# Kernel optimization log

Measured on AMD Instinct MI355X. Metric: run time of the kernel, lower is better.

The kernel has to match this reference:

```python
import jax, jax.numpy as jnp
import numpy as np

B, T, D, R, KEXP = 4, 4096, 1024, 64, 8
RH = max(D, 32)
SCALE = 0.02


def setup_inputs() -> dict:
    key = jax.random.key(0)
    ks = jax.random.split(key, 20)
    x = jax.random.normal(ks[0], (B, T, D), dtype=jnp.float32)
    W_Q = jax.random.normal(ks[1], (D, D), dtype=jnp.float32) * (1.0 / np.sqrt(D))
    W_K = jax.random.normal(ks[2], (D, D), dtype=jnp.float32) * (1.0 / np.sqrt(D))
    W_O = jax.random.normal(ks[3], (D, D), dtype=jnp.float32) * (1.0 / np.sqrt(D))
    W_inv = jnp.eye(D, dtype=jnp.float32) + 0.01 * jax.random.normal(ks[4], (D, D), dtype=jnp.float32)
    V_fwd = jax.random.normal(ks[5], (KEXP, D, R), dtype=jnp.float32) * SCALE
    W_fwd = jax.random.normal(ks[6], (KEXP, D, R), dtype=jnp.float32) * SCALE
    U_fwd = jax.random.normal(ks[7], (KEXP, D, R), dtype=jnp.float32) * SCALE
    b_fwd = jnp.zeros((KEXP, D), dtype=jnp.float32)
    V_inv = jax.random.normal(ks[8], (KEXP, D, R), dtype=jnp.float32) * SCALE
    W_inv_exp = jax.random.normal(ks[9], (KEXP, D, R), dtype=jnp.float32) * SCALE
    U_inv = jax.random.normal(ks[10], (KEXP, D, R), dtype=jnp.float32) * SCALE
    b_inv = jnp.zeros((KEXP, D), dtype=jnp.float32)
    router_w1 = jax.random.normal(ks[11], (RH, D), dtype=jnp.float32) * (1.0 / np.sqrt(D))
    router_b1 = jnp.zeros((RH,), dtype=jnp.float32)
    router_w2 = jax.random.normal(ks[12], (KEXP, RH), dtype=jnp.float32) * (1.0 / np.sqrt(RH))
    router_b2 = jnp.zeros((KEXP,), dtype=jnp.float32)
    alpha_bi = jnp.asarray(0.5, dtype=jnp.float32)
    expert_bias = jnp.zeros((KEXP,), dtype=jnp.float32)
    return dict(x=x, W_Q=W_Q, W_K=W_K, W_O=W_O, W_inv=W_inv,
                V_fwd=V_fwd, W_fwd=W_fwd, U_fwd=U_fwd, b_fwd=b_fwd,
                V_inv=V_inv, W_inv_exp=W_inv_exp, U_inv=U_inv, b_inv=b_inv,
                router_w1=router_w1, router_b1=router_b1,
                router_w2=router_w2, router_b2=router_b2,
                alpha_bi=alpha_bi, expert_bias=expert_bias)


def _fused_branch(Q_side, K_side, V, W, U, b, router_w1, router_b1, router_w2, router_b2, expert_bias):
    # Q_side, K_side: (B,T,D); V,W,U: (K,D,r); b: (K,D)
    xV = jnp.einsum('btd,kdr->btkr', Q_side, V)          # (B,T,K,r)
    yW = jnp.einsum('btd,kdr->btkr', K_side, W)          # (B,T,K,r)
    cum_yW = jnp.cumsum(yW, axis=1)                      # causal prefix sum over T
    prod = xV * cum_yW
    # query-side router: Linear -> GELU(exact) -> Linear, plus balance bias
    h = jax.nn.gelu(Q_side @ router_w1.T + router_b1, approximate=False)
    logits = h @ router_w2.T + router_b2 + expert_bias
    weights = jax.nn.softmax(logits, axis=-1)            # (B,T,K)
    out = jnp.einsum('btkr,kdr->btd', prod * weights[..., None], U)
    out = out + weights @ b
    n_valid = jnp.arange(1, Q_side.shape[1] + 1, dtype=Q_side.dtype)
    return out / n_valid[None, :, None]


def reference(x, W_Q, W_K, W_O, W_inv,
              V_fwd, W_fwd, U_fwd, b_fwd,
              V_inv, W_inv_exp, U_inv, b_inv,
              router_w1, router_b1, router_w2, router_b2,
              alpha_bi, expert_bias):
    Q = x @ W_Q.T
    K = x @ W_K.T
    invQ = Q @ W_inv.T
    invK = K @ W_inv.T
    fwd = _fused_branch(Q, K, V_fwd, W_fwd, U_fwd, b_fwd,
                        router_w1, router_b1, router_w2, router_b2, expert_bias)
    inv = _fused_branch(invQ, invK, W_inv_exp, V_inv, U_inv, b_inv,
                        router_w1, router_b1, router_w2, router_b2, expert_bias)
    out = fwd + alpha_bi * inv
    return out @ W_O.T
```

## Files before the change

kernel.cpp:

```cpp
#include <hip/hip_runtime.h>
#include <hip/hip_bf16.h>
#include <math.h>

#define BDIM 1024
#define TDIM 4096
#define BT   16384
#define KEXPN 8
#define RRANK 64
#define KR   512
#define KC   640
#define PW   1280
#define KRC  1024
#define NCH  64
#define TC   64

typedef __attribute__((ext_vector_type(8))) short bf16x8;
typedef __attribute__((ext_vector_type(4))) float f32x4;

typedef __attribute__((address_space(1))) char g_char;
typedef __attribute__((address_space(3))) char l_char;

__device__ __forceinline__ void gload16(const short* g, short* lds_base_uniform) {
  __builtin_amdgcn_global_load_lds((const g_char*)(const char*)g,
                                   (l_char*)(char*)lds_base_uniform, 16, 0, 0);
}

__global__ __launch_bounds__(256) void cvt_bf16_kernel(const float* __restrict__ in,
    __hip_bfloat16* __restrict__ out, long n4) {
  long id = (long)blockIdx.x * 256 + threadIdx.x;
  if (id >= n4) return;
  f32x4 v = ((const f32x4*)in)[id];
  long i = id * 4;
  out[i + 0] = __float2bfloat16(v[0]);
  out[i + 1] = __float2bfloat16(v[1]);
  out[i + 2] = __float2bfloat16(v[2]);
  out[i + 3] = __float2bfloat16(v[3]);
}

__global__ __launch_bounds__(256) void transpose3_kernel(
    const float* __restrict__ in0, __hip_bfloat16* __restrict__ o0,
    const float* __restrict__ in1, __hip_bfloat16* __restrict__ o1,
    const float* __restrict__ in2, __hip_bfloat16* __restrict__ o2) {
  int id = blockIdx.x * 256 + threadIdx.x;
  if (id >= BDIM * BDIM) return;
  const float* in = blockIdx.y == 0 ? in0 : (blockIdx.y == 1 ? in1 : in2);
  __hip_bfloat16* out = blockIdx.y == 0 ? o0 : (blockIdx.y == 1 ? o1 : o2);
  int d = id & (BDIM - 1);
  int e = id >> 10;
  out[(size_t)e * BDIM + d] = __float2bfloat16(in[(size_t)d * BDIM + e]);
}

__global__ __launch_bounds__(256) void vmat4_kernel(
    const float* __restrict__ i0, __hip_bfloat16* __restrict__ o0,
    const float* __restrict__ i1, __hip_bfloat16* __restrict__ o1,
    const float* __restrict__ i2, __hip_bfloat16* __restrict__ o2,
    const float* __restrict__ i3, __hip_bfloat16* __restrict__ o3) {
  int id = blockIdx.x * 256 + threadIdx.x;
  if (id >= KR * BDIM) return;
  const float* V = blockIdx.y == 0 ? i0 : (blockIdx.y == 1 ? i1 : (blockIdx.y == 2 ? i2 : i3));
  __hip_bfloat16* out = blockIdx.y == 0 ? o0 : (blockIdx.y == 1 ? o1 : (blockIdx.y == 2 ? o2 : o3));
  int d = id & (BDIM - 1);
  int kr = id >> 10;
  int k = kr >> 6, r = kr & 63;
  out[(size_t)kr * BDIM + d] = __float2bfloat16(V[((size_t)k * BDIM + d) * RRANK + r]);
}

__global__ __launch_bounds__(256) void utT2_kernel(
    const float* __restrict__ U0, const float* __restrict__ b0, __hip_bfloat16* __restrict__ o0,
    const float* __restrict__ U1, const float* __restrict__ b1, __hip_bfloat16* __restrict__ o1) {
  int id = blockIdx.x * 256 + threadIdx.x;
  if (id >= KC * BDIM) return;
  const float* U = blockIdx.y ? U1 : U0;
  const float* bvec = blockIdx.y ? b1 : b0;
  __hip_bfloat16* out = blockIdx.y ? o1 : o0;
  int e = id & (BDIM - 1);
  int c = id >> 10;
  float v = 0.0f;
  if (c < KR) {
    int k = c >> 6, r = c & 63;
    v = U[((size_t)k * BDIM + e) * RRANK + r];
  } else if (c < KR + KEXPN) {
    v = bvec[(size_t)(c - KR) * BDIM + e];
  }
  out[(size_t)c * BDIM + e] = __float2bfloat16(v);
}

__global__ __launch_bounds__(256) void gemm_fold(const __hip_bfloat16* __restrict__ A,
    const __hip_bfloat16* __restrict__ B, void* __restrict__ C1, void* __restrict__ C2,
    void* __restrict__ C3, int rs1, int rs2, int ldc, int M, int N, int Kd) {
  __shared__ __align__(16) short Als[2][128 * 32];
  __shared__ __align__(16) short Bls[2][128 * 32];
  int nbx = gridDim.x;
  int nwg = nbx * gridDim.y;
  int bx = blockIdx.x, by = blockIdx.y;
  if ((nwg & 7) == 0) {
    int orig = by * nbx + bx;
    int cpx = nwg >> 3;
    int id = (orig & 7) * cpx + (orig >> 3);
    bx = id % nbx; by = id / nbx;
  }
  const short* As = (const short*)A;
  const short* Bs = (const short*)B;
  const int t  = threadIdx.x;
  const int w  = t >> 6;
  const int l  = t & 63;
  const int lr = l & 15;
  const int lk = l >> 4;
  const int wr = w >> 1;
  const int wc = w & 1;
  const int row0 = by * 128;
  const int col0 = bx * 128;
  const int srow = w * 16 + (l >> 2);
  const int scol = (l & 3) * 8;
  const short* ag0 = As + (size_t)(row0 + srow) * Kd + scol;
  const short* ag1 = As + (size_t)(row0 + 64 + srow) * Kd + scol;
  const short* bg0 = Bs + (size_t)(col0 + srow) * Kd + scol;
  const short* bg1 = Bs + (size_t)(col0 + 64 + srow) * Kd + scol;
  f32x4 acc[4][4] = {};
  const int nt = Kd / 32;
  auto stage = [&](int kt, int buf) {
    int k0 = kt * 32;
    gload16(ag0 + k0, &Als[buf][w * 512]);
    gload16(ag1 + k0, &Als[buf][2048 + w * 512]);
    gload16(bg0 + k0, &Bls[buf][w * 512]);
    gload16(bg1 + k0, &Bls[buf][2048 + w * 512]);
  };
  stage(0, 0);
  __syncthreads();
  int cur = 0;
  for (int kt = 0; kt < nt; ++kt) {
    if (kt + 1 < nt) stage(kt + 1, cur ^ 1);
    bf16x8 af[4], bfr[4];
    #pragma unroll
    for (int i = 0; i < 4; i++)
      af[i] = *(const bf16x8*)&Als[cur][(wr * 64 + i * 16 + lr) * 32 + lk * 8];
    #pragma unroll
    for (int j = 0; j < 4; j++)
      bfr[j] = *(const bf16x8*)&Bls[cur][(wc * 64 + j * 16 + lr) * 32 + lk * 8];
    #pragma unroll
    for (int i = 0; i < 4; i++)
      #pragma unroll
      for (int j = 0; j < 4; j++)
        acc[i][j] = __builtin_amdgcn_mfma_f32_16x16x32_bf16(af[i], bfr[j], acc[i][j], 0, 0, 0);
    __syncthreads();
    cur ^= 1;
  }
  #pragma unroll
  for (int i = 0; i < 4; i++)
    #pragma unroll
    for (int j = 0; j < 4; j++)
      #pragma unroll
      for (int g = 0; g < 4; g++) {
        int r = row0 + wr * 64 + i * 16 + lk * 4 + g;
        int c = col0 + wc * 64 + j * 16 + lr;
        void* dst = C1; int rr = r;
        if (r >= rs2)      { dst = C3; rr = r - rs2; }
        else if (r >= rs1) { dst = C2; rr = r - rs1; }
        ((__hip_bfloat16*)dst)[(size_t)rr * ldc + c] = __float2bfloat16(acc[i][j][g]);
      }
}

template<int EPI>
__global__ __launch_bounds__(512, 2) void gemm_nt_256(const __hip_bfloat16* __restrict__ A,
    const __hip_bfloat16* __restrict__ B, void* __restrict__ Cv, void* __restrict__ Cv2,
    int csplit, int ldc, int ldc2, const float* __restrict__ bias, int M, int N, int Kd) {
  __shared__ __align__(16) short Als[2][2][256 * 32];
  __shared__ __align__(16) short Bls[2][2][256 * 32];

  int nbx = gridDim.x;
  int nwg = nbx * gridDim.y;
  int bx = blockIdx.x, by = blockIdx.y;
  if ((nwg & 7) == 0) {
    int orig = by * nbx + bx;
    int cpx = nwg >> 3;
    int id = (orig & 7) * cpx + (orig >> 3);
    bx = id % nbx; by = id / nbx;
  }
  const short* As = (const short*)A;
  const short* Bs = (const short*)B;
  const int t  = threadIdx.x;
  const int w  = t >> 6;
  const int l  = t & 63;
  const int lr = l & 15;
  const int lk = l >> 4;
  const int wr = w >> 2;
  const int wc = w & 3;
  const int row0 = by * 256;
  const int col0 = bx * 256;

  const int srow  = t >> 2;
  const int sslot = (t & 3) ^ ((srow >> 1) & 3);
  const short* agA0 = As + (size_t)(row0 + srow) * Kd + sslot * 8;
  const short* agA1 = As + (size_t)(row0 + 128 + srow) * Kd + sslot * 8;
  const short* bgB0 = Bs + (size_t)(col0 + srow) * Kd + sslot * 8;
  const short* bgB1 = Bs + (size_t)(col0 + 128 + srow) * Kd + sslot * 8;

  auto stageA = [&](int buf, int kh, int kt) {
    int k0 = kt * 64 + kh * 32;
    short* base = &Als[buf][kh][0];
    gload16(agA0 + k0, base + w * 512);
    gload16(agA1 + k0, base + 4096 + w * 512);
  };
  auto stageB = [&](int buf, int kh, int kt) {
    int k0 = kt * 64 + kh * 32;
    short* base = &Bls[buf][kh][0];
    gload16(bgB0 + k0, base + w * 512);
    gload16(bgB1 + k0, base + 4096 + w * 512);
  };

  int aoff[8], boff[4];
  #pragma unroll
  for (int mf = 0; mf < 8; ++mf) {
    int r = wr * 128 + mf * 16 + lr;
    aoff[mf] = r * 32 + ((lk ^ ((r >> 1) & 3)) << 3);
  }
  #pragma unroll
  for (int nf = 0; nf < 4; ++nf) {
    int r = wc * 64 + nf * 16 + lr;
    boff[nf] = r * 32 + ((lk ^ ((r >> 1) & 3)) << 3);
  }

  f32x4 acc[8][4] = {};
  const int NT = Kd >> 6;

  stageA(0, 0, 0); stageA(0, 1, 0); stageB(0, 0, 0); stageB(0, 1, 0);
  asm volatile("s_waitcnt vmcnt(0)" ::: "memory");
  __builtin_amdgcn_sched_barrier(0);
  __builtin_amdgcn_s_barrier();

  for (int kt = 0; kt < NT; ++kt) {
    const int buf = kt & 1, nb = buf ^ 1;
    const short* A0 = &Als[buf][0][0];
    const short* A1 = &Als[buf][1][0];
    const short* B0 = &Bls[buf][0][0];
    const short* B1 = &Bls[buf][1][0];
    const bool st = (kt + 1 < NT);
    bf16x8 af[4], bfr[4];

    #pragma unroll
    for (int i = 0; i < 4; ++i) bfr[i] = *(const bf16x8*)&B0[boff[i]];
    #pragma unroll
    for (int i = 0; i < 4; ++i) af[i]  = *(const bf16x8*)&A0[aoff[i]];
    if (st) { stageA(nb, 0, kt + 1); stageA(nb, 1, kt + 1); }
    __builtin_amdgcn_s_barrier();
    __builtin_amdgcn_s_setprio(1);
    #pragma unroll
    for (int i = 0; i < 4; ++i)
      #pragma unroll
      for (int j = 0; j < 4; ++j)
        acc[i][j] = __builtin_amdgcn_mfma_f32_16x16x32_bf16(af[i], bfr[j], acc[i][j], 0, 0, 0);
    __builtin_amdgcn_s_setprio(0);
    __builtin_amdgcn_s_barrier();

    #pragma unroll
    for (int i = 0; i < 4; ++i) af[i] = *(const bf16x8*)&A0[aoff[4 + i]];
    if (st) { stageB(nb, 0, kt + 1); stageB(nb, 1, kt + 1); }
    __builtin_amdgcn_s_barrier();
    __builtin_amdgcn_s_setprio(1);
    #pragma unroll
    for (int i = 0; i < 4; ++i)
      #pragma unroll
      for (int j = 0; j < 4; ++j)
        acc[4 + i][j] = __builtin_amdgcn_mfma_f32_16x16x32_bf16(af[i], bfr[j], acc[4 + i][j], 0, 0, 0);
    __builtin_amdgcn_s_setprio(0);
    __builtin_amdgcn_s_barrier();

    #pragma unroll
    for (int i = 0; i < 4; ++i) bfr[i] = *(const bf16x8*)&B1[boff[i]];
    #pragma unroll
    for (int i = 0; i < 4; ++i) af[i]  = *(const bf16x8*)&A1[aoff[i]];
    __builtin_amdgcn_s_barrier();
    __builtin_amdgcn_s_setprio(1);
    #pragma unroll
    for (int i = 0; i < 4; ++i)
      #pragma unroll
      for (int j = 0; j < 4; ++j)
        acc[i][j] = __builtin_amdgcn_mfma_f32_16x16x32_bf16(af[i], bfr[j], acc[i][j], 0, 0, 0);
    __builtin_amdgcn_s_setprio(0);
    __builtin_amdgcn_s_barrier();

    #pragma unroll
    for (int i = 0; i < 4; ++i) af[i] = *(const bf16x8*)&A1[aoff[4 + i]];
    __builtin_amdgcn_s_barrier();
    __builtin_amdgcn_s_setprio(1);
    #pragma unroll
    for (int i = 0; i < 4; ++i)
      #pragma unroll
      for (int j = 0; j < 4; ++j)
        acc[4 + i][j] = __builtin_amdgcn_mfma_f32_16x16x32_bf16(af[i], bfr[j], acc[4 + i][j], 0, 0, 0);
    __builtin_amdgcn_s_setprio(0);
    asm volatile("s_waitcnt vmcnt(0)" ::: "memory");
    __builtin_amdgcn_sched_barrier(0);
    __builtin_amdgcn_s_barrier();
  }

  #pragma unroll
  for (int mf = 0; mf < 8; ++mf)
    #pragma unroll
    for (int nf = 0; nf < 4; ++nf)
      #pragma unroll
      for (int g = 0; g < 4; ++g) {
        int r = row0 + wr * 128 + mf * 16 + lk * 4 + g;
        int c = col0 + wc * 64 + nf * 16 + lr;
        float v = acc[mf][nf][g];
        void* dst = Cv;
        int cc = c, ld = ldc;
        if (c >= csplit) { dst = Cv2; cc = c - csplit; ld = ldc2; }
        size_t idx = (size_t)r * ld + cc;
        if (EPI == 0)      ((float*)dst)[idx] = v;
        else if (EPI == 1) ((__hip_bfloat16*)dst)[idx] = __float2bfloat16(v);
        else if (EPI == 2) {
          float xv = v + bias[cc];
          float gl = 0.5f * xv * (1.0f + erff(xv * 0.70710678118654752f));
          ((__hip_bfloat16*)dst)[idx] = __float2bfloat16(gl);
        } else {
          float s = 1.0f / (float)((r & (TDIM - 1)) + 1);
          ((float*)dst)[idx] = v * s;
        }
      }
}

__global__ __launch_bounds__(256) void router_kernel(const __hip_bfloat16* __restrict__ Hf,
    const __hip_bfloat16* __restrict__ Hi,
    const float* __restrict__ w2, const float* __restrict__ b2,
    const float* __restrict__ ebias, float* __restrict__ wgt_f, float* __restrict__ wgt_i) {
  const __hip_bfloat16* H = blockIdx.y ? Hi : Hf;
  float* wgt = blockIdx.y ? wgt_i : wgt_f;
  int wv = threadIdx.x >> 6;
  int l  = threadIdx.x & 63;
  int row = blockIdx.x * 4 + wv;
  if (row >= BT) return;
  const short* Hs = (const short*)H;
  float acc[KEXPN] = {};
  #pragma unroll
  for (int i = 0; i < BDIM / 512; i++) {
    int h = (i * 64 + l) * 8;
    bf16x8 hv = *(const bf16x8*)(Hs + (size_t)row * BDIM + h);
    #pragma unroll
    for (int j = 0; j < 8; j++) {
      unsigned int ui = ((unsigned int)(unsigned short)hv[j]) << 16;
      float xv = __uint_as_float(ui);
      #pragma unroll
      for (int k = 0; k < KEXPN; k++) acc[k] += xv * w2[k * BDIM + h + j];
    }
  }
  #pragma unroll
  for (int k = 0; k < KEXPN; k++)
    for (int off = 32; off; off >>= 1) acc[k] += __shfl_down(acc[k], off);
  if (l == 0) {
    float lg[KEXPN];
    float mx = -1e30f;
    #pragma unroll
    for (int k = 0; k < KEXPN; k++) { lg[k] = acc[k] + b2[k] + ebias[k]; mx = fmaxf(mx, lg[k]); }
    float s = 0.0f;
    #pragma unroll
    for (int k = 0; k < KEXPN; k++) { lg[k] = expf(lg[k] - mx); s += lg[k]; }
    float inv = 1.0f / s;
    #pragma unroll
    for (int k = 0; k < KEXPN; k++) wgt[(size_t)row * KEXPN + k] = lg[k] * inv;
  }
}

__global__ __launch_bounds__(1024) void chunksum_kernel(const __hip_bfloat16* __restrict__ yW,
    float* __restrict__ S) {
  int j  = threadIdx.x;
  int ch = blockIdx.x;
  int b  = blockIdx.y;
  size_t base = ((size_t)b * TDIM + ch * TC) * KRC + j;
  float s = 0.0f;
  for (int t = 0; t < TC; t++) s += __bfloat162float(yW[base + (size_t)t * KRC]);
  S[((size_t)b * NCH + ch) * KRC + j] = s;
}

__global__ __launch_bounds__(1024) void scan_chunks_kernel(float* __restrict__ S) {
  int j = threadIdx.x;
  int b = blockIdx.x;
  float run = 0.0f;
  for (int ch = 0; ch < NCH; ch++) {
    size_t i = ((size_t)b * NCH + ch) * KRC + j;
    float v = S[i];
    S[i] = run;
    run += v;
  }
}

__global__ __launch_bounds__(1024) void combine_kernel(const __hip_bfloat16* __restrict__ yW,
    const float* __restrict__ S, const __hip_bfloat16* __restrict__ xV,
    const float* __restrict__ wf, const float* __restrict__ wi,
    const float* __restrict__ alphaPtr, __hip_bfloat16* __restrict__ P) {
  int j  = threadIdx.x;
  int ch = blockIdx.x;
  int b  = blockIdx.y;
  float alpha = alphaPtr[0];
  float scale = (j < KR) ? 1.0f : alpha;
  const float* wgt = (j < KR) ? wf : wi;
  int k = (j & (KR - 1)) >> 6;
  int pcol = (j < KR) ? j : j + 128;
  float run = S[((size_t)b * NCH + ch) * KRC + j];
  for (int t0 = 0; t0 < TC; t0++) {
    size_t row = (size_t)b * TDIM + ch * TC + t0;
    run += __bfloat162float(yW[row * KRC + j]);
    float p = __bfloat162float(xV[row * KRC + j]) * run * wgt[row * KEXPN + k] * scale;
    P[row * PW + pcol] = __float2bfloat16(p);
  }
  if (j < 256) {
    int half = j >> 7, jj = j & 127;
    int col = half ? (KC + KR + jj) : (KR + jj);
    const float* wg = half ? wi : wf;
    float sc = half ? alpha : 1.0f;
    for (int t0 = 0; t0 < TC; t0++) {
      size_t row = (size_t)b * TDIM + ch * TC + t0;
      float v = (jj < KEXPN) ? wg[row * KEXPN + jj] * sc : 0.0f;
      P[row * PW + col] = __float2bfloat16(v);
    }
  }
}

__global__ __launch_bounds__(256) void fill_kernel(float* __restrict__ out, long n, float val) {
  long id = (long)blockIdx.x * 256 + threadIdx.x;
  if (id < n) out[id] = val;
}

extern "C" void kernel_launch(void* const* d_in, const int* in_sizes, int n_in,
                              void* d_out, int out_size, void* d_ws, size_t ws_size,
                              hipStream_t stream) {
  const float* x        = (const float*)d_in[0];
  const float* W_Q      = (const float*)d_in[1];
  const float* W_K      = (const float*)d_in[2];
  const float* W_O      = (const float*)d_in[3];
  const float* W_inv    = (const float*)d_in[4];
  const float* V_fwd    = (const float*)d_in[5];
  const float* W_fwd    = (const float*)d_in[6];
  const float* U_fwd    = (const float*)d_in[7];
  const float* b_fwd    = (const float*)d_in[8];
  const float* V_inv    = (const float*)d_in[9];
  const float* W_inv_e  = (const float*)d_in[10];
  const float* U_inv    = (const float*)d_in[11];
  const float* b_inv    = (const float*)d_in[12];
  const float* rw1      = (const float*)d_in[13];
  const float* rb1      = (const float*)d_in[14];
  const float* rw2      = (const float*)d_in[15];
  const float* rb2      = (const float*)d_in[16];
  const float* alphaPtr = (const float*)d_in[17];
  const float* ebias    = (const float*)d_in[18];

  char* ws = (char*)d_ws;
  size_t off = 0;
  auto alloc = [&](size_t sz) -> void* {
    void* p = ws + off;
    off += (sz + 255) & ~(size_t)255;
    return p;
  };

  const size_t RB = (size_t)BDIM * 2;
  void* winvT = alloc((size_t)BDIM * RB);
  void* wqT   = alloc((size_t)BDIM * RB);
  void* wkT   = alloc((size_t)BDIM * RB);
  void* wo    = alloc((size_t)BDIM * RB);
  void* ST    = alloc((size_t)2048 * RB);
  void* HXQ   = alloc((size_t)3072 * RB);
  void* XKA   = alloc((size_t)1024 * RB);
  void* HWq   = alloc((size_t)2048 * RB);
  void* XYW   = alloc((size_t)2048 * RB);
  void* UTT   = alloc((size_t)1280 * RB);
  void* Mcat  = alloc((size_t)BDIM * PW * 2);
  void* wgt_f = alloc((size_t)BT * KEXPN * 4);
  void* wgt_i = alloc((size_t)BT * KEXPN * 4);
  void* S     = alloc((size_t)4 * NCH * KRC * 4);
  void* s_x   = alloc((size_t)BT * BDIM * 2);
  void* Hf    = alloc((size_t)BT * BDIM * 2);
  void* Hi    = alloc((size_t)BT * BDIM * 2);
  void* xVcat = alloc((size_t)BT * KRC * 2);
  void* yWcat = alloc((size_t)BT * KRC * 2);
  void* Pcat  = Hf;

  if (off > ws_size) {
    fill_kernel<<<dim3((unsigned)((out_size + 255) / 256)), 256, 0, stream>>>(
        (float*)d_out, (long)out_size, (float)(off >> 20));
    return;
  }

  __hip_bfloat16* STp  = (__hip_bfloat16*)ST;
  __hip_bfloat16* HXQp = (__hip_bfloat16*)HXQ;
  __hip_bfloat16* XKAp = (__hip_bfloat16*)XKA;
  __hip_bfloat16* XYWp = (__hip_bfloat16*)XYW;
  __hip_bfloat16* UTTp = (__hip_bfloat16*)UTT;

  auto cvt = [&](const float* in, void* out, long n) {
    long n4 = n / 4;
    cvt_bf16_kernel<<<dim3((unsigned)((n4 + 255) / 256)), dim3(256), 0, stream>>>(
        in, (__hip_bfloat16*)out, n4);
  };
  auto fold = [&](const void* A, const void* Bm, void* C1, void* C2, void* C3,
                  int rs1, int rs2, int ldc, int M, int N, int Kd) {
    dim3 g(N / 128, M / 128);
    gemm_fold<<<g, 256, 0, stream>>>((const __hip_bfloat16*)A, (const __hip_bfloat16*)Bm,
        C1, C2, C3, rs1, rs2, ldc, M, N, Kd);
  };
  auto gemm2b = [&](const void* A, const void* Bm, void* C, void* C2, int csplit,
                    int ldc, int ldc2, int M, int N, int Kd, int epi, const float* bias) {
    dim3 g(N / 256, M / 256);
    if (epi == 1)      gemm_nt_256<1><<<g, 512, 0, stream>>>((const __hip_bfloat16*)A, (const __hip_bfloat16*)Bm, C, C2, csplit, ldc, ldc2, bias, M, N, Kd);
    else if (epi == 2) gemm_nt_256<2><<<g, 512, 0, stream>>>((const __hip_bfloat16*)A, (const __hip_bfloat16*)Bm, C, C2, csplit, ldc, ldc2, bias, M, N, Kd);
    else               gemm_nt_256<4><<<g, 512, 0, stream>>>((const __hip_bfloat16*)A, (const __hip_bfloat16*)Bm, C, C2, csplit, ldc, ldc2, bias, M, N, Kd);
  };

  cvt(x,   s_x, (long)BT * BDIM);
  cvt(W_O, wo,  (long)BDIM * BDIM);
  cvt(rw1, STp,  (long)BDIM * BDIM);
  cvt(rw1, HXQp, (long)BDIM * BDIM);
  transpose3_kernel<<<dim3((BDIM * BDIM + 255) / 256, 3), 256, 0, stream>>>(
      W_inv, (__hip_bfloat16*)winvT, W_Q, (__hip_bfloat16*)wqT, W_K, (__hip_bfloat16*)wkT);
  vmat4_kernel<<<dim3((KR * BDIM + 255) / 256, 4), 256, 0, stream>>>(
      V_fwd,   HXQp + (size_t)2048 * BDIM,
      W_fwd,   XKAp,
      W_inv_e, STp + (size_t)1024 * BDIM,
      V_inv,   STp + (size_t)1536 * BDIM);
  utT2_kernel<<<dim3((KC * BDIM + 255) / 256, 2), 256, 0, stream>>>(
      U_fwd, b_fwd, UTTp, U_inv, b_inv, UTTp + (size_t)KC * BDIM);

  fold(ST, winvT, HXQp + (size_t)1024 * BDIM, HXQp + (size_t)2560 * BDIM,
       XKAp + (size_t)512 * BDIM, 1024, 1536, BDIM, 2048, BDIM, BDIM);
  fold(HXQ, wqT, HWq, XYWp, XYWp, 2048, 4096, BDIM, 3072, BDIM, BDIM);
  fold(XKA, wkT, XYWp + (size_t)1024 * BDIM, nullptr, nullptr, 1024, 2048, BDIM, 1024, BDIM, BDIM);
  fold(wo, UTT, Mcat, nullptr, nullptr, 1024, 2048, PW, BDIM, PW, BDIM);

  gemm2b(s_x, HWq, Hf, Hi, BDIM, BDIM, BDIM, BT, 2 * BDIM, BDIM, 2, rb1);
  gemm2b(s_x, XYW, xVcat, yWcat, BDIM, BDIM, BDIM, BT, 2 * BDIM, BDIM, 1, nullptr);

  router_kernel<<<dim3(BT / 4, 2), 256, 0, stream>>>((const __hip_bfloat16*)Hf,
      (const __hip_bfloat16*)Hi, rw2, rb2, ebias, (float*)wgt_f, (float*)wgt_i);

  dim3 gch(NCH, 4);
  chunksum_kernel<<<gch, 1024, 0, stream>>>((const __hip_bfloat16*)yWcat, (float*)S);
  scan_chunks_kernel<<<dim3(4), 1024, 0, stream>>>((float*)S);
  combine_kernel<<<gch, 1024, 0, stream>>>((const __hip_bfloat16*)yWcat, (const float*)S,
      (const __hip_bfloat16*)xVcat, (const float*)wgt_f, (const float*)wgt_i,
      alphaPtr, (__hip_bfloat16*)Pcat);

  gemm2b(Pcat, Mcat, d_out, d_out, BDIM, BDIM, BDIM, BT, BDIM, PW, 4, nullptr);
}
```

Baseline: 464.0 us.

## Merge fold GEMMs into paired launches and fuse x-side GEMMs into one

The four small weight-folding GEMMs are grouped into two launches, each running two independent problems over a shared flat grid. The two large x-side GEMMs (router hidden and the xV/yW projections) become one GEMM with N=4096 and a four-way segmented epilogue that applies GELU only to the first two segments. The P/Mcat layout is also compacted from 1280 to 1152 columns by packing both branches' bias-weight columns together, which shrinks the final GEMM's K dimension. This cuts launch count and padded work, at the cost of a more branchy epilogue.

```diff
diff --git a/kernel.cpp b/kernel.cpp
--- a/kernel.cpp
+++ b/kernel.cpp
@@ -8,8 +8,7 @@
 #define KEXPN 8
 #define RRANK 64
 #define KR   512
-#define KC   640
-#define PW   1280
+#define PW2  1152
 #define KRC  1024
 #define NCH  64
 #define TC   64
@@ -65,42 +64,41 @@
   out[(size_t)kr * BDIM + d] = __float2bfloat16(V[((size_t)k * BDIM + d) * RRANK + r]);
 }
 
-__global__ __launch_bounds__(256) void utT2_kernel(
-    const float* __restrict__ U0, const float* __restrict__ b0, __hip_bfloat16* __restrict__ o0,
-    const float* __restrict__ U1, const float* __restrict__ b1, __hip_bfloat16* __restrict__ o1) {
+__global__ __launch_bounds__(256) void utt_pack_kernel(
+    const float* __restrict__ Uf, const float* __restrict__ bf,
+    const float* __restrict__ Ui, const float* __restrict__ bi,
+    __hip_bfloat16* __restrict__ out) {
   int id = blockIdx.x * 256 + threadIdx.x;
-  if (id >= KC * BDIM) return;
-  const float* U = blockIdx.y ? U1 : U0;
-  const float* bvec = blockIdx.y ? b1 : b0;
-  __hip_bfloat16* out = blockIdx.y ? o1 : o0;
+  if (id >= PW2 * BDIM) return;
   int e = id & (BDIM - 1);
   int c = id >> 10;
   float v = 0.0f;
   if (c < KR) {
     int k = c >> 6, r = c & 63;
-    v = U[((size_t)k * BDIM + e) * RRANK + r];
-  } else if (c < KR + KEXPN) {
-    v = bvec[(size_t)(c - KR) * BDIM + e];
+    v = Uf[((size_t)k * BDIM + e) * RRANK + r];
+  } else if (c < 2 * KR) {
+    int c2 = c - KR;
+    int k = c2 >> 6, r = c2 & 63;
+    v = Ui[((size_t)k * BDIM + e) * RRANK + r];
+  } else if (c < 2 * KR + KEXPN) {
+    v = bf[(size_t)(c - 2 * KR) * BDIM + e];
+  } else if (c < 2 * KR + 2 * KEXPN) {
+    v = bi[(size_t)(c - 2 * KR - KEXPN) * BDIM + e];
   }
   out[(size_t)c * BDIM + e] = __float2bfloat16(v);
 }
 
-__global__ __launch_bounds__(256) void gemm_fold(const __hip_bfloat16* __restrict__ A,
-    const __hip_bfloat16* __restrict__ B, void* __restrict__ C1, void* __restrict__ C2,
-    void* __restrict__ C3, int rs1, int rs2, int ldc, int M, int N, int Kd) {
-  __shared__ __align__(16) short Als[2][128 * 32];
-  __shared__ __align__(16) short Bls[2][128 * 32];
-  int nbx = gridDim.x;
-  int nwg = nbx * gridDim.y;
-  int bx = blockIdx.x, by = blockIdx.y;
-  if ((nwg & 7) == 0) {
-    int orig = by * nbx + bx;
-    int cpx = nwg >> 3;
-    int id = (orig & 7) * cpx + (orig >> 3);
-    bx = id % nbx; by = id / nbx;
-  }
-  const short* As = (const short*)A;
-  const short* Bs = (const short*)B;
+struct FoldArgs {
+  const __hip_bfloat16* A; const __hip_bfloat16* B;
+  void* C1; void* C2; void* C3;
+  int rs1, rs2, ldc, M, N, Kd;
+};
+
+__device__ __forceinline__ void fold_body(const FoldArgs fa, int bx, int by,
+                                          short* Als, short* Bls) {
+  const short* As = (const short*)fa.A;
+  const short* Bs = (const short*)fa.B;
+  const int Kd = fa.Kd;
   const int t  = threadIdx.x;
   const int w  = t >> 6;
   const int l  = t & 63;
@@ -120,10 +118,10 @@
   const int nt = Kd / 32;
   auto stage = [&](int kt, int buf) {
     int k0 = kt * 32;
-    gload16(ag0 + k0, &Als[buf][w * 512]);
-    gload16(ag1 + k0, &Als[buf][2048 + w * 512]);
-    gload16(bg0 + k0, &Bls[buf][w * 512]);
-    gload16(bg1 + k0, &Bls[buf][2048 + w * 512]);
+    gload16(ag0 + k0, Als + buf * 4096 + w * 512);
+    gload16(ag1 + k0, Als + buf * 4096 + 2048 + w * 512);
+    gload16(bg0 + k0, Bls + buf * 4096 + w * 512);
+    gload16(bg1 + k0, Bls + buf * 4096 + 2048 + w * 512);
   };
   stage(0, 0);
   __syncthreads();
@@ -133,10 +131,10 @@
     bf16x8 af[4], bfr[4];
     #pragma unroll
     for (int i = 0; i < 4; i++)
-      af[i] = *(const bf16x8*)&Als[cur][(wr * 64 + i * 16 + lr) * 32 + lk * 8];
+      af[i] = *(const bf16x8*)&Als[cur * 4096 + (wr * 64 + i * 16 + lr) * 32 + lk * 8];
     #pragma unroll
     for (int j = 0; j < 4; j++)
-      bfr[j] = *(const bf16x8*)&Bls[cur][(wc * 64 + j * 16 + lr) * 32 + lk * 8];
+      bfr[j] = *(const bf16x8*)&Bls[cur * 4096 + (wc * 64 + j * 16 + lr) * 32 + lk * 8];
     #pragma unroll
     for (int i = 0; i < 4; i++)
       #pragma unroll
@@ -153,16 +151,31 @@
       for (int g = 0; g < 4; g++) {
         int r = row0 + wr * 64 + i * 16 + lk * 4 + g;
         int c = col0 + wc * 64 + j * 16 + lr;
-        void* dst = C1; int rr = r;
-        if (r >= rs2)      { dst = C3; rr = r - rs2; }
-        else if (r >= rs1) { dst = C2; rr = r - rs1; }
-        ((__hip_bfloat16*)dst)[(size_t)rr * ldc + c] = __float2bfloat16(acc[i][j][g]);
+        void* dst = fa.C1; int rr = r;
+        if (r >= fa.rs2)      { dst = fa.C3; rr = r - fa.rs2; }
+        else if (r >= fa.rs1) { dst = fa.C2; rr = r - fa.rs1; }
+        ((__hip_bfloat16*)dst)[(size_t)rr * fa.ldc + c] = __float2bfloat16(acc[i][j][g]);
       }
+}
+
+__global__ __launch_bounds__(256) void gemm_fold2(FoldArgs fa0, FoldArgs fa1, int nblk0) {
+  __shared__ __align__(16) short Als[2 * 128 * 32];
+  __shared__ __align__(16) short Bls[2 * 128 * 32];
+  int id = blockIdx.x;
+  if (id < nblk0) {
+    int nbx = fa0.N / 128;
+    fold_body(fa0, id % nbx, id / nbx, Als, Bls);
+  } else {
+    int lid = id - nblk0;
+    int nbx = fa1.N / 128;
+    fold_body(fa1, lid % nbx, lid / nbx, Als, Bls);
+  }
 }
 
 template<int EPI>
 __global__ __launch_bounds__(512, 2) void gemm_nt_256(const __hip_bfloat16* __restrict__ A,
     const __hip_bfloat16* __restrict__ B, void* __restrict__ Cv, void* __restrict__ Cv2,
+    void* __restrict__ Cv3, void* __restrict__ Cv4,
     int csplit, int ldc, int ldc2, const float* __restrict__ bias, int M, int N, int Kd) {
   __shared__ __align__(16) short Als[2][2][256 * 32];
   __shared__ __align__(16) short Bls[2][2][256 * 32];
@@ -303,19 +316,28 @@
         int r = row0 + wr * 128 + mf * 16 + lk * 4 + g;
         int c = col0 + wc * 64 + nf * 16 + lr;
         float v = acc[mf][nf][g];
-        void* dst = Cv;
-        int cc = c, ld = ldc;
-        if (c >= csplit) { dst = Cv2; cc = c - csplit; ld = ldc2; }
-        size_t idx = (size_t)r * ld + cc;
-        if (EPI == 0)      ((float*)dst)[idx] = v;
-        else if (EPI == 1) ((__hip_bfloat16*)dst)[idx] = __float2bfloat16(v);
-        else if (EPI == 2) {
-          float xv = v + bias[cc];
-          float gl = 0.5f * xv * (1.0f + erff(xv * 0.70710678118654752f));
-          ((__hip_bfloat16*)dst)[idx] = __float2bfloat16(gl);
+        if (EPI == 5) {
+          int seg = c >> 10;
+          int cc = c & (BDIM - 1);
+          void* dst = seg == 0 ? Cv : (seg == 1 ? Cv2 : (seg == 2 ? Cv3 : Cv4));
+          if (seg < 2) {
+            float xv = v + bias[cc];
+            v = 0.5f * xv * (1.0f + erff(xv * 0.70710678118654752f));
+          }
+          ((__hip_bfloat16*)dst)[(size_t)r * BDIM + cc] = __float2bfloat16(v);
         } else {
-          float s = 1.0f / (float)((r & (TDIM - 1)) + 1);
-          ((float*)dst)[idx] = v * s;
+          void* dst = Cv;
+          int cc = c, ld = ldc;
+          if (c >= csplit) { dst = Cv2; cc = c - csplit; ld = ldc2; }
+          size_t idx = (size_t)r * ld + cc;
+          if (EPI == 2) {
+            float xv = v + bias[cc];
+            float gl = 0.5f * xv * (1.0f + erff(xv * 0.70710678118654752f));
+            ((__hip_bfloat16*)dst)[idx] = __float2bfloat16(gl);
+          } else {
+            float s = 1.0f / (float)((r & (TDIM - 1)) + 1);
+            ((float*)dst)[idx] = v * s;
+          }
         }
       }
 }
@@ -395,23 +417,21 @@
   float scale = (j < KR) ? 1.0f : alpha;
   const float* wgt = (j < KR) ? wf : wi;
   int k = (j & (KR - 1)) >> 6;
-  int pcol = (j < KR) ? j : j + 128;
   float run = S[((size_t)b * NCH + ch) * KRC + j];
   for (int t0 = 0; t0 < TC; t0++) {
     size_t row = (size_t)b * TDIM + ch * TC + t0;
     run += __bfloat162float(yW[row * KRC + j]);
     float p = __bfloat162float(xV[row * KRC + j]) * run * wgt[row * KEXPN + k] * scale;
-    P[row * PW + pcol] = __float2bfloat16(p);
-  }
-  if (j < 256) {
-    int half = j >> 7, jj = j & 127;
-    int col = half ? (KC + KR + jj) : (KR + jj);
-    const float* wg = half ? wi : wf;
-    float sc = half ? alpha : 1.0f;
+    P[row * PW2 + j] = __float2bfloat16(p);
+  }
+  if (j < 128) {
+    int col = KRC + j;
     for (int t0 = 0; t0 < TC; t0++) {
       size_t row = (size_t)b * TDIM + ch * TC + t0;
-      float v = (jj < KEXPN) ? wg[row * KEXPN + jj] * sc : 0.0f;
-      P[row * PW + col] = __float2bfloat16(v);
+      float v = 0.0f;
+      if (j < KEXPN)          v = wf[row * KEXPN + j];
+      else if (j < 2 * KEXPN) v = wi[row * KEXPN + (j - KEXPN)] * alpha;
+      P[row * PW2 + col] = __float2bfloat16(v);
     }
   }
 }
@@ -460,10 +480,9 @@
   void* ST    = alloc((size_t)2048 * RB);
   void* HXQ   = alloc((size_t)3072 * RB);
   void* XKA   = alloc((size_t)1024 * RB);
-  void* HWq   = alloc((size_t)2048 * RB);
-  void* XYW   = alloc((size_t)2048 * RB);
-  void* UTT   = alloc((size_t)1280 * RB);
-  void* Mcat  = alloc((size_t)BDIM * PW * 2);
+  void* BigB  = alloc((size_t)4096 * RB);
+  void* UTT   = alloc((size_t)PW2 * RB);
+  void* Mcat  = alloc((size_t)BDIM * PW2 * 2);
   void* wgt_f = alloc((size_t)BT * KEXPN * 4);
   void* wgt_i = alloc((size_t)BT * KEXPN * 4);
   void* S     = alloc((size_t)4 * NCH * KRC * 4);
@@ -483,7 +502,7 @@
   __hip_bfloat16* STp  = (__hip_bfloat16*)ST;
   __hip_bfloat16* HXQp = (__hip_bfloat16*)HXQ;
   __hip_bfloat16* XKAp = (__hip_bfloat16*)XKA;
-  __hip_bfloat16* XYWp = (__hip_bfloat16*)XYW;
+  __hip_bfloat16* BigBp= (__hip_bfloat16*)BigB;
   __hip_bfloat16* UTTp = (__hip_bfloat16*)UTT;
 
   auto cvt = [&](const float* in, void* out, long n) {
@@ -491,18 +510,13 @@
     cvt_bf16_kernel<<<dim3((unsigned)((n4 + 255) / 256)), dim3(256), 0, stream>>>(
         in, (__hip_bfloat16*)out, n4);
   };
-  auto fold = [&](const void* A, const void* Bm, void* C1, void* C2, void* C3,
-                  int rs1, int rs2, int ldc, int M, int N, int Kd) {
-    dim3 g(N / 128, M / 128);
-    gemm_fold<<<g, 256, 0, stream>>>((const __hip_bfloat16*)A, (const __hip_bfloat16*)Bm,
-        C1, C2, C3, rs1, rs2, ldc, M, N, Kd);
-  };
-  auto gemm2b = [&](const void* A, const void* Bm, void* C, void* C2, int csplit,
-                    int ldc, int ldc2, int M, int N, int Kd, int epi, const float* bias) {
+  auto gemm2b = [&](const void* A, const void* Bm, void* C, void* C2, void* C3, void* C4,
+                    int csplit, int ldc, int ldc2, int M, int N, int Kd, int epi,
+                    const float* bias) {
     dim3 g(N / 256, M / 256);
-    if (epi == 1)      gemm_nt_256<1><<<g, 512, 0, stream>>>((const __hip_bfloat16*)A, (const __hip_bfloat16*)Bm, C, C2, csplit, ldc, ldc2, bias, M, N, Kd);
-    else if (epi == 2) gemm_nt_256<2><<<g, 512, 0, stream>>>((const __hip_bfloat16*)A, (const __hip_bfloat16*)Bm, C, C2, csplit, ldc, ldc2, bias, M, N, Kd);
-    else               gemm_nt_256<4><<<g, 512, 0, stream>>>((const __hip_bfloat16*)A, (const __hip_bfloat16*)Bm, C, C2, csplit, ldc, ldc2, bias, M, N, Kd);
+    if (epi == 2)      gemm_nt_256<2><<<g, 512, 0, stream>>>((const __hip_bfloat16*)A, (const __hip_bfloat16*)Bm, C, C2, C3, C4, csplit, ldc, ldc2, bias, M, N, Kd);
+    else if (epi == 5) gemm_nt_256<5><<<g, 512, 0, stream>>>((const __hip_bfloat16*)A, (const __hip_bfloat16*)Bm, C, C2, C3, C4, csplit, ldc, ldc2, bias, M, N, Kd);
+    else               gemm_nt_256<4><<<g, 512, 0, stream>>>((const __hip_bfloat16*)A, (const __hip_bfloat16*)Bm, C, C2, C3, C4, csplit, ldc, ldc2, bias, M, N, Kd);
   };
 
   cvt(x,   s_x, (long)BT * BDIM);
@@ -516,17 +530,31 @@
       W_fwd,   XKAp,
       W_inv_e, STp + (size_t)1024 * BDIM,
       V_inv,   STp + (size_t)1536 * BDIM);
-  utT2_kernel<<<dim3((KC * BDIM + 255) / 256, 2), 256, 0, stream>>>(
-      U_fwd, b_fwd, UTTp, U_inv, b_inv, UTTp + (size_t)KC * BDIM);
-
-  fold(ST, winvT, HXQp + (size_t)1024 * BDIM, HXQp + (size_t)2560 * BDIM,
-       XKAp + (size_t)512 * BDIM, 1024, 1536, BDIM, 2048, BDIM, BDIM);
-  fold(HXQ, wqT, HWq, XYWp, XYWp, 2048, 4096, BDIM, 3072, BDIM, BDIM);
-  fold(XKA, wkT, XYWp + (size_t)1024 * BDIM, nullptr, nullptr, 1024, 2048, BDIM, 1024, BDIM, BDIM);
-  fold(wo, UTT, Mcat, nullptr, nullptr, 1024, 2048, PW, BDIM, PW, BDIM);
-
-  gemm2b(s_x, HWq, Hf, Hi, BDIM, BDIM, BDIM, BT, 2 * BDIM, BDIM, 2, rb1);
-  gemm2b(s_x, XYW, xVcat, yWcat, BDIM, BDIM, BDIM, BT, 2 * BDIM, BDIM, 1, nullptr);
+  utt_pack_kernel<<<dim3((PW2 * BDIM + 255) / 256), 256, 0, stream>>>(
+      U_fwd, b_fwd, U_inv, b_inv, UTTp);
+
+  {
+    FoldArgs f0 = { STp, (const __hip_bfloat16*)winvT,
+                    HXQp + (size_t)1024 * BDIM, HXQp + (size_t)2560 * BDIM,
+                    XKAp + (size_t)512 * BDIM, 1024, 1536, BDIM, 2048, BDIM, BDIM };
+    FoldArgs f1 = { (const __hip_bfloat16*)wo, UTTp,
+                    Mcat, nullptr, nullptr, 1 << 30, 1 << 30, PW2, BDIM, PW2, BDIM };
+    int n0 = (f0.M / 128) * (f0.N / 128);
+    int n1 = (f1.M / 128) * (f1.N / 128);
+    gemm_fold2<<<dim3(n0 + n1), 256, 0, stream>>>(f0, f1, n0);
+  }
+  {
+    FoldArgs f0 = { HXQp, (const __hip_bfloat16*)wqT,
+                    BigBp, nullptr, nullptr, 1 << 30, 1 << 30, BDIM, 3072, BDIM, BDIM };
+    FoldArgs f1 = { XKAp, (const __hip_bfloat16*)wkT,
+                    BigBp + (size_t)3072 * BDIM, nullptr, nullptr, 1 << 30, 1 << 30,
+                    BDIM, 1024, BDIM, BDIM };
+    int n0 = (f0.M / 128) * (f0.N / 128);
+    int n1 = (f1.M / 128) * (f1.N / 128);
+    gemm_fold2<<<dim3(n0 + n1), 256, 0, stream>>>(f0, f1, n0);
+  }
+
+  gemm2b(s_x, BigB, Hf, Hi, xVcat, yWcat, 0, 0, 0, BT, 4 * BDIM, BDIM, 5, rb1);
 
   router_kernel<<<dim3(BT / 4, 2), 256, 0, stream>>>((const __hip_bfloat16*)Hf,
       (const __hip_bfloat16*)Hi, rw2, rb2, ebias, (float*)wgt_f, (float*)wgt_i);
@@ -538,5 +566,6 @@
       (const __hip_bfloat16*)xVcat, (const float*)wgt_f, (const float*)wgt_i,
       alphaPtr, (__hip_bfloat16*)Pcat);
 
-  gemm2b(Pcat, Mcat, d_out, d_out, BDIM, BDIM, BDIM, BT, BDIM, PW, 4, nullptr);
-}
+  gemm2b(Pcat, Mcat, d_out, d_out, nullptr, nullptr, BDIM, BDIM, BDIM,
+         BT, BDIM, PW2, 4, nullptr);
+}
```

After: 457.9 us, median of 2. About the same (-1.3%).
